# Kernel tuning notes

Measured on AMD Instinct MI355X. Metric: run time of the kernel, lower is better.

The kernel has to match this reference:

```python
import jax, jax.numpy as jnp
import numpy as np

# SMPL-style skeleton: parent index per joint (parent < child, root = -1)
PARENTS = [-1, 0, 0, 0, 1, 2, 3, 4, 5, 6, 7, 8, 9, 9, 9, 12, 13, 14, 16, 17, 18, 19, 20, 21]
END_SITES = [10, 11, 15, 22, 23]  # feet, head, hands
NUM_JOINTS = len(PARENTS)


def rot6d_to_matrix(x):
    """6D rotation rep -> 3x3 matrix via Gram-Schmidt. x: [..., 6] -> [..., 3, 3].
    eye(3).reshape(-1)[:6] = [1,0,0,0,1,0] maps to identity under this (row-stacked) convention."""
    a1, a2 = x[..., 0:3], x[..., 3:6]
    b1 = a1 / jnp.linalg.norm(a1, axis=-1, keepdims=True)
    a2p = a2 - jnp.sum(b1 * a2, axis=-1, keepdims=True) * b1
    b2 = a2p / jnp.linalg.norm(a2p, axis=-1, keepdims=True)
    b3 = jnp.cross(b1, b2)
    return jnp.stack([b1, b2, b3], axis=-2)


def fk_positions(rot, offsets):
    """Forward kinematics (faithful to _recompute_joint_global_info).
    rot: [F, J, 3, 3] local joint rotations; offsets: [F, J, 3].
    Returns global joint positions [F, J, 3]. Loop is over the fixed, small
    joint hierarchy (structural), fully vectorized over frames."""
    positions = [offsets[:, 0]]          # root: offset only
    orientations = [rot[:, 0]]           # root: local rotation
    for i in range(1, NUM_JOINTS):
        pi = PARENTS[i]
        po = orientations[pi]            # [F, 3, 3]
        pos = jnp.einsum('fab,fb->fa', po, offsets[:, i]) + positions[pi]
        positions.append(pos)
        orientations.append(po @ rot[:, i])
    return jnp.stack(positions, axis=1)  # [F, J, 3]


def setup_inputs() -> dict:
    key = jax.random.key(0)
    ks = jax.random.split(key, 6)
    F = 65536
    return {
        'poseA': jax.random.normal(ks[0], (F, NUM_JOINTS, 6), dtype=jnp.float32),
        'poseB': jax.random.normal(ks[1], (F, NUM_JOINTS, 6), dtype=jnp.float32),
        'joint_offsets_A': jax.random.normal(ks[2], (F, NUM_JOINTS, 3), dtype=jnp.float32),
        'joint_offsets_B': jax.random.normal(ks[3], (F, NUM_JOINTS, 3), dtype=jnp.float32),
        't_poseA': jax.random.normal(ks[4], (NUM_JOINTS, 3), dtype=jnp.float32),
        't_poseB': jax.random.normal(ks[5], (NUM_JOINTS, 3), dtype=jnp.float32),
    }


def reference(poseA, poseB, joint_offsets_A, joint_offsets_B, t_poseA, t_poseB):
    ee = jnp.array(END_SITES)
    # 6D -> rotation matrices (to_matrix)
    RA = rot6d_to_matrix(poseA)
    RB = rot6d_to_matrix(poseB)
    # sequential per-joint FK (the hot loop)
    posA = fk_positions(RA, joint_offsets_A)
    posB = fk_positions(RB, joint_offsets_B)
    # bbox scale from T-pose
    scale_A = jnp.max(t_poseA, axis=0) - jnp.min(t_poseA, axis=0)  # [3]
    scale_B = jnp.max(t_poseB, axis=0) - jnp.min(t_poseB, axis=0)
    eeA = posA[:, ee, :] - t_poseA[ee, :]   # [F, E, 3]
    eeB = posB[:, ee, :] - t_poseB[ee, :]
    loss = jnp.mean((eeA / scale_A - eeB / scale_B) ** 2)
    return loss
```

## Files before the change

kernel.cpp:

```cpp
#include <hip/hip_runtime.h>


struct V3 { float x, y, z; };
struct M3 { float m[3][3]; };
struct FK { M3 o; V3 p; };

__device__ __forceinline__ V3 matvec(const M3& A, const V3& v) {
    return { A.m[0][0]*v.x + A.m[0][1]*v.y + A.m[0][2]*v.z,
             A.m[1][0]*v.x + A.m[1][1]*v.y + A.m[1][2]*v.z,
             A.m[2][0]*v.x + A.m[2][1]*v.y + A.m[2][2]*v.z };
}

__device__ __forceinline__ M3 matmul(const M3& A, const M3& B) {
    M3 C;
#pragma unroll
    for (int i = 0; i < 3; i++)
#pragma unroll
        for (int j = 0; j < 3; j++)
            C.m[i][j] = A.m[i][0]*B.m[0][j] + A.m[i][1]*B.m[1][j] + A.m[i][2]*B.m[2][j];
    return C;
}

__device__ __forceinline__ M3 rot6d(float v0, float v1, float v2,
                                    float v3, float v4, float v5) {
    float n1 = v0*v0 + v1*v1 + v2*v2;
    float r1 = 1.0f / sqrtf(n1);
    V3 b1 = { v0*r1, v1*r1, v2*r1 };
    float d = b1.x*v3 + b1.y*v4 + b1.z*v5;
    V3 u = { v3 - d*b1.x, v4 - d*b1.y, v5 - d*b1.z };
    float n2 = u.x*u.x + u.y*u.y + u.z*u.z;
    float r2 = 1.0f / sqrtf(n2);
    V3 b2 = { u.x*r2, u.y*r2, u.z*r2 };
    V3 b3 = { b1.y*b2.z - b1.z*b2.y, b1.z*b2.x - b1.x*b2.z, b1.x*b2.y - b1.y*b2.x };
    M3 R;
    R.m[0][0]=b1.x; R.m[0][1]=b1.y; R.m[0][2]=b1.z;
    R.m[1][0]=b2.x; R.m[1][1]=b2.y; R.m[1][2]=b2.z;
    R.m[2][0]=b3.x; R.m[2][1]=b3.y; R.m[2][2]=b3.z;
    return R;
}

__device__ __forceinline__ FK fk_step(float a0,float a1,float a2,float a3,float a4,float a5,
                                      float ox,float oy,float oz, const FK& par) {
    V3 t = matvec(par.o, {ox, oy, oz});
    FK s;
    s.p = { par.p.x + t.x, par.p.y + t.y, par.p.z + t.z };
    s.o = matmul(par.o, rot6d(a0, a1, a2, a3, a4, a5));
    return s;
}

__device__ __forceinline__ V3 fk_end(float ox, float oy, float oz, const FK& par) {
    V3 t = matvec(par.o, {ox, oy, oz});
    return { par.p.x + t.x, par.p.y + t.y, par.p.z + t.z };
}

#define PSTR 7
#define OSTR 5

struct SBuf { float4 p[6]; float4 o[3]; };

__device__ __forceinline__ void load_stage(SBuf& b, const float* __restrict__ P,
                                           const float* __restrict__ O,
                                           int lane, int st) {
#pragma unroll
    for (int k = 0; k < 6; k++) {
        int idx = lane + 64*k, f = idx/6, c = idx - 6*f;
        b.p[k] = *(const float4*)(P + f*144 + st*24 + c*4);
    }
#pragma unroll
    for (int k = 0; k < 3; k++) {
        int idx = lane + 64*k, f = idx/3, c = idx - 3*f;
        b.o[k] = *(const float4*)(O + f*72 + st*12 + c*4);
    }
}

__device__ __forceinline__ void write_stage(const SBuf& b, float4* sp, float4* so, int lane) {
#pragma unroll
    for (int k = 0; k < 6; k++) {
        int idx = lane + 64*k, f = idx/6, c = idx - 6*f;
        sp[f*PSTR + c] = b.p[k];
    }
#pragma unroll
    for (int k = 0; k < 3; k++) {
        int idx = lane + 64*k, f = idx/3, c = idx - 3*f;
        so[f*OSTR + c] = b.o[k];
    }
}

#define READQ  q0 = rp[0]; q1 = rp[1]; q2 = rp[2]; q3 = rp[3]; q4 = rp[4]; q5 = rp[5]; \
               r0 = ro[0]; r1 = ro[1]; r2 = ro[2];
#define J0ROT  q0.x,q0.y,q0.z,q0.w,q1.x,q1.y
#define J1ROT  q1.z,q1.w,q2.x,q2.y,q2.z,q2.w
#define J2ROT  q3.x,q3.y,q3.z,q3.w,q4.x,q4.y
#define J3ROT  q4.z,q4.w,q5.x,q5.y,q5.z,q5.w
#define J0OFF  r0.x,r0.y,r0.z
#define J1OFF  r0.w,r1.x,r1.y
#define J2OFF  r1.z,r1.w,r2.x
#define J3OFF  r2.y,r2.z,r2.w

__global__ __launch_bounds__(256, 2)
void ee_loss_kernel(const float* __restrict__ poseA, const float* __restrict__ poseB,
                    const float* __restrict__ offA,  const float* __restrict__ offB,
                    const float* __restrict__ tA,    const float* __restrict__ tB,
                    float* __restrict__ out, float inv_count) {
    __shared__ float4 s_pose[4][64 * PSTR];
    __shared__ float4 s_off [4][64 * OSTR];
    __shared__ float s_eeB[128][15];
    __shared__ float s_inv[6];
    __shared__ float s_d[15];
    __shared__ float s_part[2];

    const int tid  = threadIdx.x;
    const int wid  = tid >> 6;
    const int lane = tid & 63;
    const bool isB = wid & 1;
    const int fg   = wid >> 1;
    const int fl   = fg * 64 + lane;
    const long long f0 = (long long)blockIdx.x * 128 + fg * 64;

    const float* __restrict__ P = (isB ? poseB : poseA) + f0 * 144;
    const float* __restrict__ O = (isB ? offB  : offA ) + f0 * 72;

    float4* sp = s_pose[wid];
    float4* so = s_off[wid];
    const float4* rp = sp + lane * PSTR;
    const float4* ro = so + lane * OSTR;

    SBuf bA, bB;
    load_stage(bA, P, O, lane, 0);
    load_stage(bB, P, O, lane, 1);

    if (tid < 6) {
        const float* tp = (tid < 3) ? tA : tB;
        int ax = (tid < 3) ? tid : tid - 3;
        float mn = tp[ax], mx = mn;
#pragma unroll
        for (int j = 1; j < 24; j++) {
            float v = tp[j*3 + ax];
            mn = fminf(mn, v); mx = fmaxf(mx, v);
        }
        s_inv[tid] = 1.0f / (mx - mn);
    }
    if (tid < 15) {
        const int EE[5] = {10, 11, 15, 22, 23};
        int e = tid / 3, ax = tid - 3*e;
        int j = EE[e];
        float mnA = tA[ax], mxA = mnA, mnB = tB[ax], mxB = mnB;
#pragma unroll
        for (int k = 1; k < 24; k++) {
            float a = tA[k*3 + ax], b = tB[k*3 + ax];
            mnA = fminf(mnA, a); mxA = fmaxf(mxA, a);
            mnB = fminf(mnB, b); mxB = fmaxf(mxB, b);
        }
        s_d[tid] = tB[j*3 + ax]/(mxB - mnB) - tA[j*3 + ax]/(mxA - mnA);
    }

    write_stage(bA, sp, so, lane);

    float4 q0, q1, q2, q3, q4, q5, r0, r1, r2;

    READQ;
    load_stage(bA, P, O, lane, 2);
    FK s0; s0.o = rot6d(J0ROT); s0.p = { r0.x, r0.y, r0.z };
    FK s1 = fk_step(J1ROT, J1OFF, s0);
    FK s2 = fk_step(J2ROT, J2OFF, s0);
    FK s3 = fk_step(J3ROT, J3OFF, s0);
    write_stage(bB, sp, so, lane);

    READQ;
    load_stage(bB, P, O, lane, 3);
    FK s4 = fk_step(J0ROT, J0OFF, s1);
    FK s5 = fk_step(J1ROT, J1OFF, s2);
    FK s6 = fk_step(J2ROT, J2OFF, s3);
    FK s7 = fk_step(J3ROT, J3OFF, s4);
    write_stage(bA, sp, so, lane);

    READQ;
    load_stage(bA, P, O, lane, 4);
    FK s8 = fk_step(J0ROT, J0OFF, s5);
    FK s9 = fk_step(J1ROT, J1OFF, s6);
    V3 e10 = fk_end(J2OFF, s7);
    V3 e11 = fk_end(J3OFF, s8);
    write_stage(bB, sp, so, lane);

    READQ;
    load_stage(bB, P, O, lane, 5);
    FK s12 = fk_step(J0ROT, J0OFF, s9);
    FK s13 = fk_step(J1ROT, J1OFF, s9);
    FK s14 = fk_step(J2ROT, J2OFF, s9);
    V3 e15 = fk_end(J3OFF, s12);
    write_stage(bA, sp, so, lane);

    READQ;
    FK s16 = fk_step(J0ROT, J0OFF, s13);
    FK s17 = fk_step(J1ROT, J1OFF, s14);
    FK s18 = fk_step(J2ROT, J2OFF, s16);
    FK s19 = fk_step(J3ROT, J3OFF, s17);
    write_stage(bB, sp, so, lane);

    READQ;
    FK s20 = fk_step(J0ROT, J0OFF, s18);
    FK s21 = fk_step(J1ROT, J1OFF, s19);
    V3 e22 = fk_end(J2OFF, s20);
    V3 e23 = fk_end(J3OFF, s21);

    if (isB) {
        s_eeB[fl][ 0] = e10.x; s_eeB[fl][ 1] = e10.y; s_eeB[fl][ 2] = e10.z;
        s_eeB[fl][ 3] = e11.x; s_eeB[fl][ 4] = e11.y; s_eeB[fl][ 5] = e11.z;
        s_eeB[fl][ 6] = e15.x; s_eeB[fl][ 7] = e15.y; s_eeB[fl][ 8] = e15.z;
        s_eeB[fl][ 9] = e22.x; s_eeB[fl][10] = e22.y; s_eeB[fl][11] = e22.z;
        s_eeB[fl][12] = e23.x; s_eeB[fl][13] = e23.y; s_eeB[fl][14] = e23.z;
    }
    __syncthreads();

    float local = 0.0f;
    if (!isB) {
        const float iax = s_inv[0], iay = s_inv[1], iaz = s_inv[2];
        const float ibx = s_inv[3], iby = s_inv[4], ibz = s_inv[5];
        const float* eb = s_eeB[fl];
        float t0  = e10.x*iax - eb[ 0]*ibx + s_d[ 0];
        float t1  = e10.y*iay - eb[ 1]*iby + s_d[ 1];
        float t2  = e10.z*iaz - eb[ 2]*ibz + s_d[ 2];
        float t3  = e11.x*iax - eb[ 3]*ibx + s_d[ 3];
        float t4  = e11.y*iay - eb[ 4]*iby + s_d[ 4];
        float t5  = e11.z*iaz - eb[ 5]*ibz + s_d[ 5];
        float t6  = e15.x*iax - eb[ 6]*ibx + s_d[ 6];
        float t7  = e15.y*iay - eb[ 7]*iby + s_d[ 7];
        float t8  = e15.z*iaz - eb[ 8]*ibz + s_d[ 8];
        float t9  = e22.x*iax - eb[ 9]*ibx + s_d[ 9];
        float t10 = e22.y*iay - eb[10]*iby + s_d[10];
        float t11 = e22.z*iaz - eb[11]*ibz + s_d[11];
        float t12 = e23.x*iax - eb[12]*ibx + s_d[12];
        float t13 = e23.y*iay - eb[13]*iby + s_d[13];
        float t14 = e23.z*iaz - eb[14]*ibz + s_d[14];
        local = ((t0*t0 + t1*t1) + (t2*t2 + t3*t3) + (t4*t4 + t5*t5) +
                 (t6*t6 + t7*t7) + (t8*t8 + t9*t9) + (t10*t10 + t11*t11) +
                 (t12*t12 + t13*t13) + t14*t14) * inv_count;
#pragma unroll
        for (int off = 32; off > 0; off >>= 1)
            local += __shfl_down(local, off, 64);
        if (lane == 0) s_part[fg] = local;
    }
    __syncthreads();
    if (tid == 0) atomicAdd(out, s_part[0] + s_part[1]);
}

extern "C" void kernel_launch(void* const* d_in, const int* in_sizes, int n_in,
                              void* d_out, int out_size, void* d_ws, size_t ws_size,
                              hipStream_t stream) {
    const float* poseA = (const float*)d_in[0];
    const float* poseB = (const float*)d_in[1];
    const float* offA  = (const float*)d_in[2];
    const float* offB  = (const float*)d_in[3];
    const float* tA    = (const float*)d_in[4];
    const float* tB    = (const float*)d_in[5];
    float* out = (float*)d_out;

    const int F = in_sizes[0] / 144;
    const int blocks = F / 128;
    const float inv_count = 1.0f / ((float)F * 15.0f);

    hipMemsetAsync(out, 0, sizeof(float), stream);
    ee_loss_kernel<<<blocks, 256, 0, stream>>>(poseA, poseB, offA, offB, tA, tB,
                                               out, inv_count);
}
```

Measured before the change: 172.8 us.

## Stream pose and offset stages directly into LDS with global_load_lds double buffering

Replaces the register-staged load-then-write pipeline with direct global-to-LDS loads (global_load_lds, 16 bytes) into two per-wave LDS buffers, using explicit vmcnt/lgkmcnt waits to overlap the next stage's fetch with FK compute. This removes the VGPRs held for in-flight stages and the ds_write instructions, and drops the occupancy hint from launch_bounds. The end-effector scratch now aliases the offset buffers behind an extra barrier. It relies on hand-placed waitcnt values, and the unpadded LDS layout may raise bank conflicts on the per-lane reads.

Result: faster. 149.2 us (-13.6%).

```diff
diff --git a/kernel.cpp b/kernel.cpp
--- a/kernel.cpp
+++ b/kernel.cpp
@@ -53,41 +53,30 @@
     return { par.p.x + t.x, par.p.y + t.y, par.p.z + t.z };
 }
 
-#define PSTR 7
-#define OSTR 5
-
-struct SBuf { float4 p[6]; float4 o[3]; };
-
-__device__ __forceinline__ void load_stage(SBuf& b, const float* __restrict__ P,
-                                           const float* __restrict__ O,
-                                           int lane, int st) {
-#pragma unroll
-    for (int k = 0; k < 6; k++) {
-        int idx = lane + 64*k, f = idx/6, c = idx - 6*f;
-        b.p[k] = *(const float4*)(P + f*144 + st*24 + c*4);
-    }
-#pragma unroll
-    for (int k = 0; k < 3; k++) {
-        int idx = lane + 64*k, f = idx/3, c = idx - 3*f;
-        b.o[k] = *(const float4*)(O + f*72 + st*12 + c*4);
-    }
-}
-
-__device__ __forceinline__ void write_stage(const SBuf& b, float4* sp, float4* so, int lane) {
-#pragma unroll
-    for (int k = 0; k < 6; k++) {
-        int idx = lane + 64*k, f = idx/6, c = idx - 6*f;
-        sp[f*PSTR + c] = b.p[k];
-    }
-#pragma unroll
-    for (int k = 0; k < 3; k++) {
-        int idx = lane + 64*k, f = idx/3, c = idx - 3*f;
-        so[f*OSTR + c] = b.o[k];
-    }
-}
-
-#define READQ  q0 = rp[0]; q1 = rp[1]; q2 = rp[2]; q3 = rp[3]; q4 = rp[4]; q5 = rp[5]; \
-               r0 = ro[0]; r1 = ro[1]; r2 = ro[2];
+#define GLDS16(gp, lp) __builtin_amdgcn_global_load_lds( \
+    (const __attribute__((address_space(1))) void*)(gp), \
+    (__attribute__((address_space(3))) void*)(lp), 16, 0, 0)
+
+#define VWAIT(n) do { asm volatile("s_waitcnt vmcnt(" #n ")" ::: "memory"); \
+                      __builtin_amdgcn_sched_barrier(0); } while (0)
+#define LWAIT0()  do { asm volatile("s_waitcnt lgkmcnt(0)" ::: "memory"); \
+                      __builtin_amdgcn_sched_barrier(0); } while (0)
+
+__device__ __forceinline__ void stage(const float* __restrict__ P,
+                                      const float* __restrict__ O,
+                                      const int* pOfs, const int* oOfs,
+                                      float4* pbuf, float4* obuf, int st) {
+#pragma unroll
+    for (int k = 0; k < 6; k++)
+        GLDS16(P + st*24 + pOfs[k], pbuf + 64*k);
+#pragma unroll
+    for (int k = 0; k < 3; k++)
+        GLDS16(O + st*12 + oOfs[k], obuf + 64*k);
+}
+
+#define READQ(pb, ob) \
+    q0 = (pb)[0]; q1 = (pb)[1]; q2 = (pb)[2]; q3 = (pb)[3]; q4 = (pb)[4]; q5 = (pb)[5]; \
+    r0 = (ob)[0]; r1 = (ob)[1]; r2 = (ob)[2];
 #define J0ROT  q0.x,q0.y,q0.z,q0.w,q1.x,q1.y
 #define J1ROT  q1.z,q1.w,q2.x,q2.y,q2.z,q2.w
 #define J2ROT  q3.x,q3.y,q3.z,q3.w,q4.x,q4.y
@@ -97,17 +86,17 @@
 #define J2OFF  r1.z,r1.w,r2.x
 #define J3OFF  r2.y,r2.z,r2.w
 
-__global__ __launch_bounds__(256, 2)
+__global__ __launch_bounds__(256)
 void ee_loss_kernel(const float* __restrict__ poseA, const float* __restrict__ poseB,
                     const float* __restrict__ offA,  const float* __restrict__ offB,
                     const float* __restrict__ tA,    const float* __restrict__ tB,
                     float* __restrict__ out, float inv_count) {
-    __shared__ float4 s_pose[4][64 * PSTR];
-    __shared__ float4 s_off [4][64 * OSTR];
-    __shared__ float s_eeB[128][15];
+    __shared__ float4 s_pose[4][2][64*6];
+    __shared__ float4 s_off [4][2][64*3];
     __shared__ float s_inv[6];
     __shared__ float s_d[15];
     __shared__ float s_part[2];
+    float* s_eeB = (float*)&s_off[0][0][0];
 
     const int tid  = threadIdx.x;
     const int wid  = tid >> 6;
@@ -120,14 +109,14 @@
     const float* __restrict__ P = (isB ? poseB : poseA) + f0 * 144;
     const float* __restrict__ O = (isB ? offB  : offA ) + f0 * 72;
 
-    float4* sp = s_pose[wid];
-    float4* so = s_off[wid];
-    const float4* rp = sp + lane * PSTR;
-    const float4* ro = so + lane * OSTR;
-
-    SBuf bA, bB;
-    load_stage(bA, P, O, lane, 0);
-    load_stage(bB, P, O, lane, 1);
+    float4* pb0 = &s_pose[wid][0][0];
+    float4* pb1 = &s_pose[wid][1][0];
+    float4* ob0 = &s_off[wid][0][0];
+    float4* ob1 = &s_off[wid][1][0];
+    const float4* rp0 = pb0 + lane * 6;
+    const float4* rp1 = pb1 + lane * 6;
+    const float4* ro0 = ob0 + lane * 3;
+    const float4* ro1 = ob1 + lane * 3;
 
     if (tid < 6) {
         const float* tp = (tid < 3) ? tA : tB;
@@ -154,61 +143,81 @@
         s_d[tid] = tB[j*3 + ax]/(mxB - mnB) - tA[j*3 + ax]/(mxA - mnA);
     }
 
-    write_stage(bA, sp, so, lane);
+    int pOfs[6], oOfs[3];
+#pragma unroll
+    for (int k = 0; k < 6; k++) {
+        int idx = lane + 64*k, f = idx/6, c = idx - 6*f;
+        pOfs[k] = f*144 + c*4;
+    }
+#pragma unroll
+    for (int k = 0; k < 3; k++) {
+        int idx = lane + 64*k, f = idx/3, c = idx - 3*f;
+        oOfs[k] = f*72 + c*4;
+    }
+
+    stage(P, O, pOfs, oOfs, pb0, ob0, 0);
+    stage(P, O, pOfs, oOfs, pb1, ob1, 1);
 
     float4 q0, q1, q2, q3, q4, q5, r0, r1, r2;
 
-    READQ;
-    load_stage(bA, P, O, lane, 2);
+    VWAIT(9);
+    READQ(rp0, ro0);
+    LWAIT0();
+    stage(P, O, pOfs, oOfs, pb0, ob0, 2);
     FK s0; s0.o = rot6d(J0ROT); s0.p = { r0.x, r0.y, r0.z };
     FK s1 = fk_step(J1ROT, J1OFF, s0);
     FK s2 = fk_step(J2ROT, J2OFF, s0);
     FK s3 = fk_step(J3ROT, J3OFF, s0);
-    write_stage(bB, sp, so, lane);
-
-    READQ;
-    load_stage(bB, P, O, lane, 3);
+
+    VWAIT(9);
+    READQ(rp1, ro1);
+    LWAIT0();
+    stage(P, O, pOfs, oOfs, pb1, ob1, 3);
     FK s4 = fk_step(J0ROT, J0OFF, s1);
     FK s5 = fk_step(J1ROT, J1OFF, s2);
     FK s6 = fk_step(J2ROT, J2OFF, s3);
     FK s7 = fk_step(J3ROT, J3OFF, s4);
-    write_stage(bA, sp, so, lane);
-
-    READQ;
-    load_stage(bA, P, O, lane, 4);
+
+    VWAIT(9);
+    READQ(rp0, ro0);
+    LWAIT0();
+    stage(P, O, pOfs, oOfs, pb0, ob0, 4);
     FK s8 = fk_step(J0ROT, J0OFF, s5);
     FK s9 = fk_step(J1ROT, J1OFF, s6);
     V3 e10 = fk_end(J2OFF, s7);
     V3 e11 = fk_end(J3OFF, s8);
-    write_stage(bB, sp, so, lane);
-
-    READQ;
-    load_stage(bB, P, O, lane, 5);
+
+    VWAIT(9);
+    READQ(rp1, ro1);
+    LWAIT0();
+    stage(P, O, pOfs, oOfs, pb1, ob1, 5);
     FK s12 = fk_step(J0ROT, J0OFF, s9);
     FK s13 = fk_step(J1ROT, J1OFF, s9);
     FK s14 = fk_step(J2ROT, J2OFF, s9);
     V3 e15 = fk_end(J3OFF, s12);
-    write_stage(bA, sp, so, lane);
-
-    READQ;
+
+    VWAIT(9);
+    READQ(rp0, ro0);
     FK s16 = fk_step(J0ROT, J0OFF, s13);
     FK s17 = fk_step(J1ROT, J1OFF, s14);
     FK s18 = fk_step(J2ROT, J2OFF, s16);
     FK s19 = fk_step(J3ROT, J3OFF, s17);
-    write_stage(bB, sp, so, lane);
-
-    READQ;
+
+    VWAIT(0);
+    READQ(rp1, ro1);
     FK s20 = fk_step(J0ROT, J0OFF, s18);
     FK s21 = fk_step(J1ROT, J1OFF, s19);
     V3 e22 = fk_end(J2OFF, s20);
     V3 e23 = fk_end(J3OFF, s21);
 
+    __syncthreads();
     if (isB) {
-        s_eeB[fl][ 0] = e10.x; s_eeB[fl][ 1] = e10.y; s_eeB[fl][ 2] = e10.z;
-        s_eeB[fl][ 3] = e11.x; s_eeB[fl][ 4] = e11.y; s_eeB[fl][ 5] = e11.z;
-        s_eeB[fl][ 6] = e15.x; s_eeB[fl][ 7] = e15.y; s_eeB[fl][ 8] = e15.z;
-        s_eeB[fl][ 9] = e22.x; s_eeB[fl][10] = e22.y; s_eeB[fl][11] = e22.z;
-        s_eeB[fl][12] = e23.x; s_eeB[fl][13] = e23.y; s_eeB[fl][14] = e23.z;
+        float* eb = s_eeB + fl * 15;
+        eb[ 0] = e10.x; eb[ 1] = e10.y; eb[ 2] = e10.z;
+        eb[ 3] = e11.x; eb[ 4] = e11.y; eb[ 5] = e11.z;
+        eb[ 6] = e15.x; eb[ 7] = e15.y; eb[ 8] = e15.z;
+        eb[ 9] = e22.x; eb[10] = e22.y; eb[11] = e22.z;
+        eb[12] = e23.x; eb[13] = e23.y; eb[14] = e23.z;
     }
     __syncthreads();
 
@@ -216,7 +225,7 @@
     if (!isB) {
         const float iax = s_inv[0], iay = s_inv[1], iaz = s_inv[2];
         const float ibx = s_inv[3], iby = s_inv[4], ibz = s_inv[5];
-        const float* eb = s_eeB[fl];
+        const float* eb = s_eeB + fl * 15;
         float t0  = e10.x*iax - eb[ 0]*ibx + s_d[ 0];
         float t1  = e10.y*iay - eb[ 1]*iby + s_d[ 1];
         float t2  = e10.z*iaz - eb[ 2]*ibz + s_d[ 2];
```
